# Performance work log

Hardware: AMD Instinct MI355X
Metric: run time of the kernel (lower is better)

## Reference

```python
import jax, jax.numpy as jnp
import numpy as np

B, L, DIM = 8, 512, 8          # batch, seq len, raw channels (value dim D = 2*DIM = 16)
ET, HID, H = 128, 128, 2       # embed_time, hidden_size, num_heads
MAXLEN = 512
NEG = -1e9


def setup_inputs() -> dict:
    key = jax.random.key(0)
    ks = jax.random.split(key, 40)
    def n(i, shape, s=0.05):
        return jax.random.normal(ks[i], shape, jnp.float32) * s
    vals = jax.random.normal(ks[0], (B, L, DIM), jnp.float32)
    msk = (jax.random.uniform(ks[1], (B, L, DIM)) > 0.2).astype(jnp.float32)
    x = jnp.concatenate([vals, msk], -1)                      # (B, L, 2*DIM)
    time_steps = jax.random.uniform(ks[2], (B, L), jnp.float32)
    return {
        'x': x, 'time_steps': time_steps,
        # learned time embedding: Linear(1, ET-1) periodic + Linear(1,1)
        'w_per': n(3, (1, ET - 1)), 'b_per': n(4, (ET - 1,)),
        'w_lin': n(5, (1, 1)), 'b_lin': n(6, (1,)),
        # MultiTimeAttention projections
        'Wq_t': n(7, (ET, ET)), 'bq_t': n(8, (ET,)),
        'Wk_t': n(9, (ET, ET)), 'bk_t': n(10, (ET,)),
        'Wo_t': n(11, (2 * DIM * H, HID)), 'bo_t': n(12, (HID,)),
        'pos_emb': n(13, (MAXLEN + 1, HID)), 'cls_emb': n(14, (1, HID)),
        # transformer block (BERT-style post-LN encoder layer, d_ff=HID)
        'tWq': n(15, (HID, HID)), 'tbq': n(16, (HID,)),
        'tWk': n(17, (HID, HID)), 'tbk': n(18, (HID,)),
        'tWv': n(19, (HID, HID)), 'tbv': n(20, (HID,)),
        'tWo': n(21, (HID, HID)), 'tbo': n(22, (HID,)),
        'ln1_g': jnp.ones((HID,), jnp.float32), 'ln1_b': jnp.zeros((HID,), jnp.float32),
        'fW1': n(23, (HID, HID)), 'fb1': n(24, (HID,)),
        'fW2': n(25, (HID, HID)), 'fb2': n(26, (HID,)),
        'ln2_g': jnp.ones((HID,), jnp.float32), 'ln2_b': jnp.zeros((HID,), jnp.float32),
        # BertPooler
        'pW': n(27, (HID, HID)), 'pb': n(28, (HID,)),
    }


def _time_emb(tt, w_per, b_per, w_lin, b_lin):
    tt = tt[..., None]                                        # (B, L, 1)
    return jnp.concatenate([tt @ w_lin + b_lin, jnp.sin(tt @ w_per + b_per)], -1)


def _ln(x, g, b, eps=1e-5):
    m = x.mean(-1, keepdims=True)
    v = ((x - m) ** 2).mean(-1, keepdims=True)
    return (x - m) / jnp.sqrt(v + eps) * g + b


def _mta(q_emb, k_emb, value, mask, Wq, bq, Wk, bk, Wo, bo):
    # MultiTimeAttention: scores broadcast to value-channel axis, softmax over keys
    D = value.shape[-1]
    dk = ET // H
    def split(e, W, b):
        p = e @ W + b
        return p.reshape(e.shape[0], -1, H, dk).transpose(0, 2, 1, 3)
    q = split(q_emb, Wq, bq)                                  # (Bq, H, Lq, dk)
    k = split(k_emb, Wk, bk)                                  # (B,  H, Lk, dk)
    scores = jnp.matmul(q, k.swapaxes(-1, -2)) / jnp.sqrt(jnp.float32(dk))  # (B,H,Lq,Lk)
    s5 = jnp.where(mask[:, None, None, :, :] == 0, NEG, scores[..., None])  # (B,H,Lq,Lk,D)
    p = jax.nn.softmax(s5, axis=-2)
    out = jnp.einsum('bhqkd,bkd->bhqd', p, value)             # (B, H, Lq, D)
    Bv = value.shape[0]
    out = out.transpose(0, 2, 1, 3).reshape(Bv, -1, H * D)
    return out @ Wo + bo


def _tblock(x, tWq, tbq, tWk, tbk, tWv, tbv, tWo, tbo, ln1_g, ln1_b,
            fW1, fb1, fW2, fb2, ln2_g, ln2_b):
    Bq, Lq, _ = x.shape
    dk = HID // H
    def heads(W, b):
        return (x @ W + b).reshape(Bq, Lq, H, dk).transpose(0, 2, 1, 3)
    q, k, v = heads(tWq, tbq), heads(tWk, tbk), heads(tWv, tbv)
    a = jax.nn.softmax(jnp.matmul(q, k.swapaxes(-1, -2)) / jnp.sqrt(jnp.float32(dk)), -1)
    o = jnp.matmul(a, v).transpose(0, 2, 1, 3).reshape(Bq, Lq, HID) @ tWo + tbo
    x = _ln(x + o, ln1_g, ln1_b)
    f = jax.nn.relu(x @ fW1 + fb1) @ fW2 + fb2
    return _ln(x + f, ln2_g, ln2_b)


def reference(x, time_steps, w_per, b_per, w_lin, b_lin,
              Wq_t, bq_t, Wk_t, bk_t, Wo_t, bo_t, pos_emb, cls_emb,
              tWq, tbq, tWk, tbk, tWv, tbv, tWo, tbo, ln1_g, ln1_b,
              fW1, fb1, fW2, fb2, ln2_g, ln2_b, pW, pb):
    Bx = x.shape[0]
    mask_half = x[:, :, DIM:]
    mask = jnp.concatenate([mask_half, mask_half], -1)        # (B, L, 2*DIM)
    key_e = _time_emb(time_steps, w_per, b_per, w_lin, b_lin)
    tq_e = _time_emb(time_steps, w_per, b_per, w_lin, b_lin)  # query_time_steps=None -> same
    cls_t = jnp.linspace(0.0, 1.0, 128, dtype=jnp.float32)[None]
    cls_q_e = _time_emb(cls_t, w_per, b_per, w_lin, b_lin)    # (1, 128, ET)
    cls_out = _mta(cls_q_e, key_e, x, mask, Wq_t, bq_t, Wk_t, bk_t, Wo_t, bo_t)
    out = _mta(tq_e, key_e, x, mask, Wq_t, bq_t, Wk_t, bk_t, Wo_t, bo_t)
    tb = (tWq, tbq, tWk, tbk, tWv, tbv, tWo, tbo, ln1_g, ln1_b,
          fW1, fb1, fW2, fb2, ln2_g, ln2_b)
    cls_repr = jnp.broadcast_to(cls_emb[None, :, :], (Bx, 1, HID))
    # encode(cls_out, is_pooling=True), pooling='bert': no pos emb, take token 0
    h = _tblock(jnp.concatenate([cls_repr, cls_out], 1), *tb)
    cls_pooling = jnp.tanh(h[:, 0] @ pW + pb)                 # (B, HID)
    # encode(out, is_pooling=False) [pretrain path]: pos emb + transformer, drop CLS
    h2 = jnp.concatenate([cls_repr, out], 1)                  # (B, L+1, HID)
    h2 = h2 + pos_emb[:h2.shape[1]][None]
    h2 = _tblock(h2, *tb)
    last_hidden_state = h2[:, 1:]                             # (B, L, HID)
    return cls_pooling, last_hidden_state
```

## Files before the change

kernel.cpp:

```cpp
#include <hip/hip_runtime.h>
#include <hip/hip_bf16.h>
#include <math.h>


static constexpr int NM_ = 8 * 513;
static constexpr int NC_ = 8 * 129;
static constexpr int NT_ = NM_ + NC_;
static constexpr int VTS_ = 5248;

using bf = __hip_bfloat16;
typedef __attribute__((ext_vector_type(8))) short bf16x8;
typedef __attribute__((ext_vector_type(4))) short bf16x4;
typedef __attribute__((ext_vector_type(4))) float floatx4;
typedef __attribute__((ext_vector_type(8))) unsigned short ushortx8;

__device__ __forceinline__ float wave_reduce_sum(float v) {
    #pragma unroll
    for (int off = 32; off >= 1; off >>= 1) v += __shfl_xor(v, off);
    return v;
}
__device__ __forceinline__ float wave_reduce_max(float v) {
    #pragma unroll
    for (int off = 32; off >= 1; off >>= 1) v = fmaxf(v, __shfl_xor(v, off));
    return v;
}
__device__ __forceinline__ float u2f(unsigned short u) {
    return __uint_as_float(((unsigned)u) << 16);
}
__device__ __forceinline__ unsigned short f2u(float f) {
    unsigned u = __float_as_uint(f);
    return (unsigned short)((u + 0x7FFF + ((u >> 16) & 1)) >> 16);
}
__device__ __forceinline__ bf16x8 join8(bf16x4 lo, bf16x4 hi) {
    return __builtin_shufflevector(lo, hi, 0, 1, 2, 3, 4, 5, 6, 7);
}
__device__ __forceinline__ float rdin(const void* p, int i, int flag) {
    return flag ? u2f(((const unsigned short*)p)[i]) : ((const float*)p)[i];
}

struct PrepAll {
    const void* src[32]; int n[32]; int dstoff[32];
    int cstart[32]; int cnum[32];
    int ncv;
    const void* wsrc[8]; unsigned short* wdst[8]; float wscale[8];
    const void* ts; const void* w_per; const void* b_per;
    const void* w_lin; const void* b_lin;
    unsigned short* key_e16;
    unsigned short* btg;
    const void* xsrc;
    unsigned short* vt;
    const unsigned short* det;
};
__global__ void prep_all_kernel(PrepAll a, float* dst) {
    int flag = (a.det[0] == 0x3F80u) ? 1 : 0;
    int blk = blockIdx.x, tid = threadIdx.x;
    if (blk < a.ncv) {
        int which = -1, bi = 0;
        #pragma unroll
        for (int i = 0; i < 32; ++i)
            if (blk >= a.cstart[i] && blk < a.cstart[i] + a.cnum[i]) { which = i; bi = blk - a.cstart[i]; }
        if (which < 0) return;
        int i = bi * 256 + tid;
        if (i < a.n[which]) dst[a.dstoff[which] + i] = rdin(a.src[which], i, flag);
    } else if (blk < a.ncv + 512) {
        int p = blk - a.ncv;
        int m = p >> 6;
        int idx = (p & 63) * 256 + tid;
        int c = idx >> 9;
        int l = (idx >> 3) & 63;
        int j = idx & 7;
        int k = (c >> 3) * 32 + (l >> 4) * 8 + j;
        int n = (c & 7) * 16 + (l & 15);
        a.wdst[m][idx] = f2u(rdin(a.wsrc[m], k * 128 + n, flag) * a.wscale[m]);
    } else if (blk < a.ncv + 512 + 2112) {
        int p = blk - a.ncv - 512;
        int row = p * 2 + (tid >> 7), j = tid & 127;
        float t = (row < 4096) ? rdin(a.ts, row, flag)
                               : (float)(row - 4096) * (1.0f / 127.0f);
        float v;
        if (j == 0) v = t * rdin(a.w_lin, 0, flag) + rdin(a.b_lin, 0, flag);
        else        v = sinf(t * rdin(a.w_per, j - 1, flag) + rdin(a.b_per, j - 1, flag));
        a.key_e16[row * 128 + j] = f2u(v);
    } else if (blk < a.ncv + 512 + 2112 + 32) {
        int p = blk - a.ncv - 512 - 2112;
        int e0 = (p * 256 + tid) * 8;
        int b = e0 >> 13;
        int c = (e0 >> 9) & 15;
        int k0 = e0 & 511;
        unsigned short out[8];
        #pragma unroll
        for (int j = 0; j < 8; ++j) {
            int k = k0 + j;
            float m = rdin(a.xsrc, (b * 512 + k) * 16 + 8 + (c & 7), flag);
            float val = (c < 8) ? rdin(a.xsrc, (b * 512 + k) * 16 + c, flag) * m : m;
            out[j] = f2u(val);
        }
        *(ushortx8*)(a.btg + e0) = *(ushortx8*)out;
    } else {
        int p = blk - a.ncv - 512 - 2112 - 32;
        int idx = p * 256 + tid;
        if (idx < 128 * 14) {
            int n = idx / 14, c8 = idx - n * 14;
            ushortx8 z = {0, 0, 0, 0, 0, 0, 0, 0};
            *(ushortx8*)(a.vt + (size_t)n * VTS_ + 5136 + c8 * 8) = z;
        }
    }
}

struct GemmM {
    const void* A[3]; const unsigned short* W[3]; const float* bias[3];
    unsigned short* C[3];
    int M[3]; float bscale[3];
};
__global__ void __launch_bounds__(256)
gemm_mfma_kernel(GemmM p) {
    int y = blockIdx.y;
    const unsigned short* Wsw = p.W[y];
    const float* bias = p.bias[y];
    unsigned short* C = p.C[y];
    int M = p.M[y];
    float bscale = p.bscale[y];
    int m0 = blockIdx.x * 16;
    if (m0 >= M) return;
    int tid = threadIdx.x;
    int wv = tid >> 6, lane = tid & 63;
    int am = lane & 15, aq = lane >> 4;
    const unsigned short* A = (const unsigned short*)p.A[y];
    const unsigned short* Arow = A + (size_t)(m0 + am) * 128;
    floatx4 acc0 = {0.f, 0.f, 0.f, 0.f}, acc1 = acc0;
    #pragma unroll
    for (int ks = 0; ks < 4; ++ks) {
        bf16x8 af = *(const bf16x8*)(Arow + ks * 32 + aq * 8);
        const unsigned short* base = Wsw + ((size_t)ks * 8 + 2 * wv) * 512 + lane * 8;
        bf16x8 b0 = *(const bf16x8*)(base);
        bf16x8 b1 = *(const bf16x8*)(base + 512);
        acc0 = __builtin_amdgcn_mfma_f32_16x16x32_bf16(af, b0, acc0, 0, 0, 0);
        acc1 = __builtin_amdgcn_mfma_f32_16x16x32_bf16(af, b1, acc1, 0, 0, 0);
    }
    int col = lane & 15, rowb = (lane >> 4) * 4;
    #pragma unroll
    for (int t = 0; t < 2; ++t) {
        floatx4 acc = t ? acc1 : acc0;
        int n = wv * 32 + t * 16 + col;
        float bv = bias[n] * bscale;
        #pragma unroll
        for (int rg = 0; rg < 4; ++rg)
            C[(size_t)(m0 + rowb + rg) * 128 + n] = f2u(acc[rg] + bv);
    }
}

struct MaU_att { unsigned short sp[16][520]; float red[1280]; };
struct MaU_qkv { unsigned short As[16][136]; };
union MaU { MaU_att att; MaU_qkv qkv; };

__global__ void __launch_bounds__(256)
mta_fused_kernel(const unsigned short* qp_cls, const unsigned short* qp_main,
                 const unsigned short* kp, const unsigned short* btg,
                 const float* Wo, const float* bo, const float* cls_emb, const float* pos,
                 float* xin,
                 const unsigned short* Wq, const unsigned short* Wk, const unsigned short* Wv,
                 const float* bq, const float* bk, const float* bv_,
                 unsigned short* outq, unsigned short* outk, unsigned short* vT) {
    __shared__ MaU U;
    __shared__ float As32[16][36];
    int vb = blockIdx.x, tid = threadIdx.x;
    int lane = tid & 63, wv = tid >> 6;
    int m = lane & 15, g = lane >> 4;
    bool special = (vb == 320);
    int is_cls = 0, qt = 0, b = 0;
    if (!special) {
        if (vb < 256) { b = vb >> 5; qt = vb & 31; }
        else { int t = vb - 256; b = t >> 3; qt = t & 7; is_cls = 1; }
    }
    int q0 = qt * 16;

    if (!special) {
        for (int h = 0; h < 2; ++h) {
            const unsigned short* qrow = is_cls
                ? (qp_cls + (size_t)(q0 + m) * 128 + h * 64)
                : (qp_main + (size_t)(b * 512 + q0 + m) * 128 + h * 64);
            bf16x8 qf0 = *(const bf16x8*)(qrow + g * 8);
            bf16x8 qf1 = *(const bf16x8*)(qrow + 32 + g * 8);

            const unsigned short* kbase = kp + ((size_t)b * 512) * 128 + h * 64;
            #pragma unroll
            for (int kt = 0; kt < 8; ++kt) {
                int colk = kt * 64 + wv * 16 + m;
                const unsigned short* kb = kbase + (size_t)colk * 128;
                bf16x8 b0 = *(const bf16x8*)(kb + g * 8);
                bf16x8 b1 = *(const bf16x8*)(kb + 32 + g * 8);
                floatx4 acc = {0.f, 0.f, 0.f, 0.f};
                acc = __builtin_amdgcn_mfma_f32_16x16x32_bf16(qf0, b0, acc, 0, 0, 0);
                acc = __builtin_amdgcn_mfma_f32_16x16x32_bf16(qf1, b1, acc, 0, 0, 0);
                #pragma unroll
                for (int rg = 0; rg < 4; ++rg) U.att.sp[g * 4 + rg][colk] = f2u(acc[rg]);
            }
            __syncthreads();

            for (int rr = wv; rr < 16; rr += 4) {
                float mx = -1e30f;
                for (int k = lane; k < 512; k += 64) mx = fmaxf(mx, u2f(U.att.sp[rr][k]));
                mx = wave_reduce_max(mx);
                for (int k = lane; k < 512; k += 64)
                    U.att.sp[rr][k] = f2u(expf(u2f(U.att.sp[rr][k]) - mx));
            }
            __syncthreads();

            floatx4 macc = {0.f, 0.f, 0.f, 0.f};
            {
                const unsigned short* bbase = btg + ((size_t)(b * 16 + m)) * 512 + g * 8;
                #pragma unroll
                for (int cc = 0; cc < 4; ++cc) {
                    int koff = (wv + cc * 4) * 32;
                    bf16x8 af = *(const bf16x8*)&U.att.sp[m][koff + g * 8];
                    bf16x8 bfv = *(const bf16x8*)(bbase + koff);
                    macc = __builtin_amdgcn_mfma_f32_16x16x32_bf16(af, bfv, macc, 0, 0, 0);
                }
            }
            float* redC = U.att.red;
            float* Cfull = U.att.red + 1024;
            #pragma unroll
            for (int rg = 0; rg < 4; ++rg) redC[tid * 4 + rg] = macc[rg];
            __syncthreads();
            {
                int l = tid >> 2, rg = tid & 3;
                float s = redC[l * 4 + rg] + redC[(64 + l) * 4 + rg]
                        + redC[(128 + l) * 4 + rg] + redC[(192 + l) * 4 + rg];
                int row = (l >> 4) * 4 + rg, c = l & 15;
                Cfull[row * 16 + c] = s;
            }
            __syncthreads();
            if (tid < 128) {
                int r = tid >> 3, c = tid & 7;
                float num = Cfull[r * 16 + c];
                float den = Cfull[r * 16 + 8 + c];
                As32[r][h * 16 + c] = num / den;
                As32[r][h * 16 + 8 + c] = 1.0f;
            }
            __syncthreads();
        }
    }

    int r = tid >> 4, gi = tid & 15, c0 = gi * 8;
    int segbase = is_cls ? (NM_ + b * 129) : (b * 513);
    auto Rof = [&](int rr) -> int {
        if (special) return (rr < 8) ? rr * 513 : NM_ + (rr - 8) * 129;
        return segbase + 1 + q0 + rr;
    };
    int R = Rof(r);
    int prow;
    if (special) prow = (r < 8) ? 0 : -1;
    else prow = is_cls ? -1 : (1 + q0 + r);

    float acc[8];
    if (special) {
        #pragma unroll
        for (int j = 0; j < 8; ++j) acc[j] = cls_emb[c0 + j];
    } else {
        #pragma unroll
        for (int j = 0; j < 8; ++j) acc[j] = bo[c0 + j];
        #pragma unroll 8
        for (int k = 0; k < 32; ++k) {
            float a = As32[r][k];
            const float4 w0 = *(const float4*)(Wo + (size_t)k * 128 + c0);
            const float4 w1 = *(const float4*)(Wo + (size_t)k * 128 + c0 + 4);
            acc[0] = fmaf(a, w0.x, acc[0]); acc[1] = fmaf(a, w0.y, acc[1]);
            acc[2] = fmaf(a, w0.z, acc[2]); acc[3] = fmaf(a, w0.w, acc[3]);
            acc[4] = fmaf(a, w1.x, acc[4]); acc[5] = fmaf(a, w1.y, acc[5]);
            acc[6] = fmaf(a, w1.z, acc[6]); acc[7] = fmaf(a, w1.w, acc[7]);
        }
    }
    if (prow >= 0) {
        const float* pr = pos + (size_t)prow * 128 + c0;
        float4 p0 = *(const float4*)(pr);
        float4 p1 = *(const float4*)(pr + 4);
        acc[0] += p0.x; acc[1] += p0.y; acc[2] += p0.z; acc[3] += p0.w;
        acc[4] += p1.x; acc[5] += p1.y; acc[6] += p1.z; acc[7] += p1.w;
    }
    *(float4*)(xin + (size_t)R * 128 + c0) = make_float4(acc[0], acc[1], acc[2], acc[3]);
    *(float4*)(xin + (size_t)R * 128 + c0 + 4) = make_float4(acc[4], acc[5], acc[6], acc[7]);
    *(ushort4*)&U.qkv.As[r][c0] = make_ushort4(f2u(acc[0]), f2u(acc[1]), f2u(acc[2]), f2u(acc[3]));
    *(ushort4*)&U.qkv.As[r][c0 + 4] = make_ushort4(f2u(acc[4]), f2u(acc[5]), f2u(acc[6]), f2u(acc[7]));
    __syncthreads();

    int am = lane & 15, aq = lane >> 4;
    int col = lane & 15, rowb = (lane >> 4) * 4;
    const unsigned short* Ws[3] = {Wq, Wk, Wv};
    const float* bs[3] = {bq, bk, bv_};
    float bsc[3] = {0.125f, 1.f, 1.f};
    unsigned short* Cs[2] = {outq, outk};
    #pragma unroll
    for (int y = 0; y < 3; ++y) {
        floatx4 acc0 = {0.f, 0.f, 0.f, 0.f}, acc1 = acc0;
        #pragma unroll
        for (int ks = 0; ks < 4; ++ks) {
            bf16x8 af = *(bf16x8*)&U.qkv.As[am][ks * 32 + aq * 8];
            const unsigned short* base = Ws[y] + ((size_t)ks * 8 + 2 * wv) * 512 + lane * 8;
            bf16x8 b0 = *(const bf16x8*)(base);
            bf16x8 b1 = *(const bf16x8*)(base + 512);
            acc0 = __builtin_amdgcn_mfma_f32_16x16x32_bf16(af, b0, acc0, 0, 0, 0);
            acc1 = __builtin_amdgcn_mfma_f32_16x16x32_bf16(af, b1, acc1, 0, 0, 0);
        }
        #pragma unroll
        for (int t = 0; t < 2; ++t) {
            floatx4 a2 = t ? acc1 : acc0;
            int n = wv * 32 + t * 16 + col;
            float bvv = bs[y][n] * bsc[y];
            #pragma unroll
            for (int rg = 0; rg < 4; ++rg) {
                unsigned short val = f2u(a2[rg] + bvv);
                int R2 = Rof(rowb + rg);
                if (y < 2) Cs[y][(size_t)R2 * 128 + n] = val;
                else       vT[(size_t)n * VTS_ + R2] = val;
            }
        }
    }
}

struct TbU_att { unsigned short sp[16][588]; };
struct TbU_ffn { float Xs[16][128]; unsigned short Hs[16][136]; };
union TbU { TbU_att att; TbU_ffn ffn; };

__global__ void __launch_bounds__(256)
tb_fused_kernel(const unsigned short* qp, const unsigned short* kp,
                const unsigned short* vT, const float* resid,
                const unsigned short* Wao, const float* bao,
                const float* g1, const float* b1ln,
                const unsigned short* W1, const float* fb1,
                const unsigned short* W2, const float* fb2,
                const float* g2, const float* b2ln,
                const float* pW, const float* pb, float* dout) {
    __shared__ TbU U;
    __shared__ unsigned short As[16][136];
    __shared__ float rinv[16];
    __shared__ float redS[4][4][4], redQ[4][4][4], smean[16], sinv[16], x2row[128];
    __shared__ int poolb;

    int xx = blockIdx.x, b = blockIdx.y, tid = threadIdx.x;
    int is_cls = (xx >= 33);
    int qt = is_cls ? xx - 33 : xx;
    int Lq = is_cls ? 129 : 513;
    int base = is_cls ? (NM_ + b * 129) : (b * 513);
    int nkt = is_cls ? 3 : 9;
    int lane = tid & 63, wv = tid >> 6;
    int q0 = qt * 16, m = lane & 15, g = lane >> 4;
    if (tid == 0) poolb = -1;

    for (int h = 0; h < 2; ++h) {
        int qr = q0 + m; if (qr >= Lq) qr = Lq - 1;
        const unsigned short* qrow = qp + (size_t)(base + qr) * 128 + h * 64;
        bf16x8 qf0 = *(const bf16x8*)(qrow + g * 8);
        bf16x8 qf1 = *(const bf16x8*)(qrow + 32 + g * 8);

        for (int kt = 0; kt < nkt; ++kt) {
            int colk = kt * 64 + wv * 16 + m;
            int krow = (colk < Lq) ? colk : (Lq - 1);
            const unsigned short* kb = kp + (size_t)(base + krow) * 128 + h * 64;
            bf16x8 b0 = *(const bf16x8*)(kb + g * 8);
            bf16x8 b1 = *(const bf16x8*)(kb + 32 + g * 8);
            floatx4 acc = {0.f, 0.f, 0.f, 0.f};
            acc = __builtin_amdgcn_mfma_f32_16x16x32_bf16(qf0, b0, acc, 0, 0, 0);
            acc = __builtin_amdgcn_mfma_f32_16x16x32_bf16(qf1, b1, acc, 0, 0, 0);
            #pragma unroll
            for (int rg = 0; rg < 4; ++rg)
                U.att.sp[g * 4 + rg][colk] = f2u((colk < Lq) ? acc[rg] : -1e30f);
        }
        __syncthreads();

        int kend = nkt * 64;
        for (int rr = wv; rr < 16; rr += 4) {
            float mx = -1e30f;
            for (int k = lane; k < kend; k += 64) mx = fmaxf(mx, u2f(U.att.sp[rr][k]));
            mx = wave_reduce_max(mx);
            float sum = 0.f;
            for (int k = lane; k < kend; k += 64) {
                float e = expf(u2f(U.att.sp[rr][k]) - mx);
                U.att.sp[rr][k] = f2u(e);
                sum += e;
            }
            sum = wave_reduce_sum(sum);
            if (lane == 0) rinv[rr] = 1.f / sum;
        }
        __syncthreads();

        floatx4 oacc = {0.f, 0.f, 0.f, 0.f};
        const unsigned short* vbase = vT + (size_t)(h * 64 + wv * 16 + m) * VTS_ + base;
        for (int kt = 0; kt < nkt; ++kt) {
            int k0 = kt * 64;
            #pragma unroll
            for (int c = 0; c < 2; ++c) {
                bf16x4 plo = *(const bf16x4*)&U.att.sp[m][k0 + c * 32 + g * 8];
                bf16x4 phi = *(const bf16x4*)&U.att.sp[m][k0 + c * 32 + g * 8 + 4];
                bf16x8 vf = *(const bf16x8*)(vbase + k0 + c * 32 + g * 8);
                oacc = __builtin_amdgcn_mfma_f32_16x16x32_bf16(join8(plo, phi), vf, oacc, 0, 0, 0);
            }
        }
        int dcol = wv * 16 + m;
        #pragma unroll
        for (int rg = 0; rg < 4; ++rg) {
            int q = g * 4 + rg;
            As[q][h * 64 + dcol] = f2u(oacc[rg] * rinv[q]);
        }
        __syncthreads();
    }

    int am = lane & 15, aq = lane >> 4;
    int col = lane & 15, rowb = g * 4;

    float ov[2][4];
    {
        floatx4 acc0 = {0.f, 0.f, 0.f, 0.f}, acc1 = acc0;
        #pragma unroll
        for (int ks = 0; ks < 4; ++ks) {
            bf16x8 af = *(bf16x8*)&As[am][ks * 32 + aq * 8];
            const unsigned short* wb = Wao + ((size_t)ks * 8 + 2 * wv) * 512 + lane * 8;
            bf16x8 bb0 = *(const bf16x8*)(wb);
            bf16x8 bb1 = *(const bf16x8*)(wb + 512);
            acc0 = __builtin_amdgcn_mfma_f32_16x16x32_bf16(af, bb0, acc0, 0, 0, 0);
            acc1 = __builtin_amdgcn_mfma_f32_16x16x32_bf16(af, bb1, acc1, 0, 0, 0);
        }
        #pragma unroll
        for (int t = 0; t < 2; ++t) {
            int n = wv * 32 + t * 16 + col;
            float bv = bao[n];
            floatx4 acc = t ? acc1 : acc0;
            #pragma unroll
            for (int rg = 0; rg < 4; ++rg) {
                int qo = q0 + rowb + rg;
                int rc = (qo < Lq) ? qo : (Lq - 1);
                ov[t][rg] = acc[rg] + bv + resid[(size_t)(base + rc) * 128 + n];
            }
        }
    }
    #pragma unroll
    for (int rg = 0; rg < 4; ++rg) {
        float s = ov[0][rg] + ov[1][rg];
        float q = ov[0][rg] * ov[0][rg] + ov[1][rg] * ov[1][rg];
        #pragma unroll
        for (int off = 8; off >= 1; off >>= 1) {
            s += __shfl_xor(s, off);
            q += __shfl_xor(q, off);
        }
        if ((lane & 15) == 0) { redS[wv][g][rg] = s; redQ[wv][g][rg] = q; }
    }
    __syncthreads();
    if (tid < 16) {
        int gg = tid >> 2, rg = tid & 3;
        float s = redS[0][gg][rg] + redS[1][gg][rg] + redS[2][gg][rg] + redS[3][gg][rg];
        float q = redQ[0][gg][rg] + redQ[1][gg][rg] + redQ[2][gg][rg] + redQ[3][gg][rg];
        float mean = s * 0.0078125f;
        float var = q * 0.0078125f - mean * mean;
        smean[tid] = mean;
        sinv[tid] = rsqrtf(var + 1e-5f);
    }
    __syncthreads();
    #pragma unroll
    for (int t = 0; t < 2; ++t) {
        int n = wv * 32 + t * 16 + col;
        float gm = g1[n], bb = b1ln[n];
        #pragma unroll
        for (int rg = 0; rg < 4; ++rg) {
            int row = rowb + rg;
            float val = (ov[t][rg] - smean[row]) * sinv[row] * gm + bb;
            U.ffn.Xs[row][n] = val;
            As[row][n] = f2u(val);
        }
    }
    __syncthreads();

    {
        floatx4 acc0 = {0.f, 0.f, 0.f, 0.f}, acc1 = acc0;
        #pragma unroll
        for (int ks = 0; ks < 4; ++ks) {
            bf16x8 af = *(bf16x8*)&As[am][ks * 32 + aq * 8];
            const unsigned short* wb = W1 + ((size_t)ks * 8 + 2 * wv) * 512 + lane * 8;
            bf16x8 bb0 = *(const bf16x8*)(wb);
            bf16x8 bb1 = *(const bf16x8*)(wb + 512);
            acc0 = __builtin_amdgcn_mfma_f32_16x16x32_bf16(af, bb0, acc0, 0, 0, 0);
            acc1 = __builtin_amdgcn_mfma_f32_16x16x32_bf16(af, bb1, acc1, 0, 0, 0);
        }
        #pragma unroll
        for (int t = 0; t < 2; ++t) {
            int n = wv * 32 + t * 16 + col;
            float bv = fb1[n];
            floatx4 acc = t ? acc1 : acc0;
            #pragma unroll
            for (int rg = 0; rg < 4; ++rg)
                U.ffn.Hs[rowb + rg][n] = f2u(fmaxf(acc[rg] + bv, 0.f));
        }
    }
    __syncthreads();

    floatx4 acc0 = {0.f, 0.f, 0.f, 0.f}, acc1 = acc0;
    #pragma unroll
    for (int ks = 0; ks < 4; ++ks) {
        bf16x8 af = *(bf16x8*)&U.ffn.Hs[am][ks * 32 + aq * 8];
        const unsigned short* wb = W2 + ((size_t)ks * 8 + 2 * wv) * 512 + lane * 8;
        bf16x8 bb0 = *(const bf16x8*)(wb);
        bf16x8 bb1 = *(const bf16x8*)(wb + 512);
        acc0 = __builtin_amdgcn_mfma_f32_16x16x32_bf16(af, bb0, acc0, 0, 0, 0);
        acc1 = __builtin_amdgcn_mfma_f32_16x16x32_bf16(af, bb1, acc1, 0, 0, 0);
    }
    #pragma unroll
    for (int t = 0; t < 2; ++t) {
        int n = wv * 32 + t * 16 + col;
        float bv = fb2[n];
        floatx4 acc = t ? acc1 : acc0;
        #pragma unroll
        for (int rg = 0; rg < 4; ++rg)
            ov[t][rg] = acc[rg] + bv + U.ffn.Xs[rowb + rg][n];
    }
    #pragma unroll
    for (int rg = 0; rg < 4; ++rg) {
        float s = ov[0][rg] + ov[1][rg];
        float q = ov[0][rg] * ov[0][rg] + ov[1][rg] * ov[1][rg];
        #pragma unroll
        for (int off = 8; off >= 1; off >>= 1) {
            s += __shfl_xor(s, off);
            q += __shfl_xor(q, off);
        }
        if ((lane & 15) == 0) { redS[wv][g][rg] = s; redQ[wv][g][rg] = q; }
    }
    __syncthreads();
    if (tid < 16) {
        int gg = tid >> 2, rg = tid & 3;
        float s = redS[0][gg][rg] + redS[1][gg][rg] + redS[2][gg][rg] + redS[3][gg][rg];
        float q = redQ[0][gg][rg] + redQ[1][gg][rg] + redQ[2][gg][rg] + redQ[3][gg][rg];
        float mean = s * 0.0078125f;
        float var = q * 0.0078125f - mean * mean;
        smean[tid] = mean;
        sinv[tid] = rsqrtf(var + 1e-5f);
    }
    __syncthreads();
    #pragma unroll
    for (int t = 0; t < 2; ++t) {
        int n = wv * 32 + t * 16 + col;
        float gm = g2[n], bb = b2ln[n];
        #pragma unroll
        for (int rg = 0; rg < 4; ++rg) {
            int row = rowb + rg;
            int qout = q0 + row;
            float val = (ov[t][rg] - smean[row]) * sinv[row] * gm + bb;
            if (!is_cls) {
                if (qout >= 1 && qout < Lq)
                    dout[1024 + (size_t)b * 65536 + (size_t)(qout - 1) * 128 + n] = val;
            } else {
                if (qout == 0) {
                    x2row[n] = val;
                    if (n == 0) poolb = b;
                }
            }
        }
    }
    __syncthreads();
    if (poolb >= 0 && tid < 128) {
        float acc = pb[tid];
        for (int k = 0; k < 128; ++k) acc = fmaf(x2row[k], pW[(size_t)k * 128 + tid], acc);
        dout[(size_t)poolb * 128 + tid] = tanhf(acc);
    }
}

extern "C" void kernel_launch(void* const* d_in, const int* in_sizes, int n_in,
                              void* d_out, int out_size, void* d_ws, size_t ws_size,
                              hipStream_t stream) {
    float* w = (float*)d_ws;
    size_t off = 0;
    auto alloc = [&](size_t n) {
        float* p = w + off;
        off += (n + 3) & ~(size_t)3;
        return p;
    };
    auto allocU = [&](size_t n) { return (unsigned short*)alloc((n + 1) / 2); };

    PrepAll pa{};
    int nn = n_in < 32 ? n_in : 32;
    float* fin[32];
    const int needconv[32] = {0,0,0,0,0,0, 0,1, 0,1, 1,1, 1,1, 0,1, 0,1, 0,1,
                              0,1, 1,1, 0,1, 0,1, 1,1, 1,1};
    int ncv = 0;
    for (int i = 0; i < nn; ++i) {
        pa.src[i] = d_in[i];
        pa.n[i] = in_sizes[i];
        fin[i] = alloc(in_sizes[i]);
        pa.dstoff[i] = (int)(fin[i] - w);
        if (needconv[i]) {
            int nb = (in_sizes[i] + 255) / 256;
            pa.cstart[i] = ncv;
            pa.cnum[i] = nb;
            ncv += nb;
        } else { pa.cstart[i] = -1; pa.cnum[i] = 0; }
    }
    for (int i = nn; i < 32; ++i) {
        pa.src[i] = nullptr; pa.n[i] = 0; pa.dstoff[i] = 0;
        pa.cstart[i] = -1; pa.cnum[i] = 0;
    }
    pa.ncv = ncv;

    const float* bq_t    = fin[7];
    const float* bk_t    = fin[9];
    const float* Wo_t    = fin[10]; const float* bo_t = fin[11];
    const float* pos_emb = fin[12]; const float* cls_emb = fin[13];
    const float* tbq = fin[15]; const float* tbk = fin[17]; const float* tbv = fin[19];
    const float* tbo = fin[21];
    const float* ln1_g = fin[22]; const float* ln1_b = fin[23];
    const float* fb1 = fin[25]; const float* fb2 = fin[27];
    const float* ln2_g = fin[28]; const float* ln2_b = fin[29];
    const float* pW = fin[30]; const float* pb = fin[31];

    const int widx[8] = {8, 6, 14, 16, 18, 20, 24, 26};
    unsigned short* wsw[8];
    for (int i = 0; i < 8; ++i) {
        wsw[i] = allocU(16384);
        pa.wsrc[i] = d_in[widx[i]];
        pa.wdst[i] = wsw[i];
        pa.wscale[i] = (i == 1 || i == 2) ? 0.125f : 1.0f;
    }
    pa.ts = d_in[1]; pa.w_per = d_in[2]; pa.b_per = d_in[3];
    pa.w_lin = d_in[4]; pa.b_lin = d_in[5];
    pa.xsrc = d_in[0];
    pa.det = (const unsigned short*)d_in[22];

    unsigned short* key_e16 = allocU(4224 * 128);
    unsigned short* cls_e16 = key_e16 + 4096 * 128;
    pa.key_e16 = key_e16;
    unsigned short* btg = allocU(8 * 16 * 512);
    pa.btg = btg;

    unsigned short* qp_main16 = allocU(4096 * 128);
    unsigned short* kp_main16 = allocU(4096 * 128);
    unsigned short* qp_cls16  = allocU(128 * 128);
    float* xin     = alloc((size_t)NT_ * 128);
    unsigned short* tbq16 = allocU((size_t)NT_ * 128);
    unsigned short* tbk16 = allocU((size_t)NT_ * 128);
    unsigned short* vT    = allocU((size_t)128 * VTS_);
    pa.vt = vT;
    (void)ws_size;

    float* outf = (float*)d_out;
    int prep_nblk = ncv + 512 + 2112 + 32 + 7;

    prep_all_kernel<<<prep_nblk, 256, 0, stream>>>(pa, w);

    {
        GemmM p{};
        p.A[0] = key_e16; p.W[0] = wsw[0]; p.bias[0] = bk_t; p.C[0] = kp_main16;
        p.M[0] = 4096; p.bscale[0] = 1.f;
        p.A[1] = key_e16; p.W[1] = wsw[1]; p.bias[1] = bq_t; p.C[1] = qp_main16;
        p.M[1] = 4096; p.bscale[1] = 0.125f;
        p.A[2] = cls_e16; p.W[2] = wsw[1]; p.bias[2] = bq_t; p.C[2] = qp_cls16;
        p.M[2] = 128; p.bscale[2] = 0.125f;
        gemm_mfma_kernel<<<dim3(256, 3), 256, 0, stream>>>(p);
    }

    mta_fused_kernel<<<321, 256, 0, stream>>>(qp_cls16, qp_main16, kp_main16, btg,
                                              Wo_t, bo_t, cls_emb, pos_emb, xin,
                                              wsw[2], wsw[3], wsw[4], tbq, tbk, tbv,
                                              tbq16, tbk16, vT);

    tb_fused_kernel<<<dim3(42, 8), 256, 0, stream>>>(tbq16, tbk16, vT, xin,
                                                     wsw[5], tbo, ln1_g, ln1_b,
                                                     wsw[6], fb1, wsw[7], fb2,
                                                     ln2_g, ln2_b, pW, pb, outf);
}
```

Measured before the change: 207.3 us.

## Process both attention heads together to halve barriers in fused attention kernels

Both the MTA and transformer-block attention phases now compute scores, softmax and PV products for the two heads at once, using doubled shared-memory score buffers instead of a sequential per-head loop. This cuts the number of __syncthreads per block roughly in half and exposes more independent MFMA/load work for latency hiding. The transformer path becomes templated on key-tile count, so its loops fully unroll, and both kernels add a min-blocks-per-CU launch bound of 2. The cost is larger shared memory and register use per block, which could reduce occupancy despite the launch-bound hint.

```diff
diff --git a/kernel.cpp b/kernel.cpp
--- a/kernel.cpp
+++ b/kernel.cpp
@@ -149,11 +149,10 @@
     }
 }
 
-struct MaU_att { unsigned short sp[16][520]; float red[1280]; };
-struct MaU_qkv { unsigned short As[16][136]; };
-union MaU { MaU_att att; MaU_qkv qkv; };
-
-__global__ void __launch_bounds__(256)
+struct MaAtt { unsigned short sp[2][16][520]; float red[2][1280]; };
+union MaU { MaAtt att; unsigned short qAs[16][136]; };
+
+__global__ void __launch_bounds__(256, 2)
 mta_fused_kernel(const unsigned short* qp_cls, const unsigned short* qp_main,
                  const unsigned short* kp, const unsigned short* btg,
                  const float* Wo, const float* bo, const float* cls_emb, const float* pos,
@@ -175,70 +174,89 @@
     int q0 = qt * 16;
 
     if (!special) {
+        const unsigned short* qrow = is_cls
+            ? (qp_cls + (size_t)(q0 + m) * 128)
+            : (qp_main + (size_t)(b * 512 + q0 + m) * 128);
+        bf16x8 qf[2][2];
+        #pragma unroll
         for (int h = 0; h < 2; ++h) {
-            const unsigned short* qrow = is_cls
-                ? (qp_cls + (size_t)(q0 + m) * 128 + h * 64)
-                : (qp_main + (size_t)(b * 512 + q0 + m) * 128 + h * 64);
-            bf16x8 qf0 = *(const bf16x8*)(qrow + g * 8);
-            bf16x8 qf1 = *(const bf16x8*)(qrow + 32 + g * 8);
-
-            const unsigned short* kbase = kp + ((size_t)b * 512) * 128 + h * 64;
-            #pragma unroll
-            for (int kt = 0; kt < 8; ++kt) {
-                int colk = kt * 64 + wv * 16 + m;
-                const unsigned short* kb = kbase + (size_t)colk * 128;
-                bf16x8 b0 = *(const bf16x8*)(kb + g * 8);
-                bf16x8 b1 = *(const bf16x8*)(kb + 32 + g * 8);
+            qf[h][0] = *(const bf16x8*)(qrow + h * 64 + g * 8);
+            qf[h][1] = *(const bf16x8*)(qrow + h * 64 + 32 + g * 8);
+        }
+        const unsigned short* kbase = kp + ((size_t)b * 512) * 128;
+        #pragma unroll
+        for (int kt = 0; kt < 8; ++kt) {
+            int colk = kt * 64 + wv * 16 + m;
+            const unsigned short* kb = kbase + (size_t)colk * 128;
+            #pragma unroll
+            for (int h = 0; h < 2; ++h) {
+                bf16x8 b0 = *(const bf16x8*)(kb + h * 64 + g * 8);
+                bf16x8 b1 = *(const bf16x8*)(kb + h * 64 + 32 + g * 8);
                 floatx4 acc = {0.f, 0.f, 0.f, 0.f};
-                acc = __builtin_amdgcn_mfma_f32_16x16x32_bf16(qf0, b0, acc, 0, 0, 0);
-                acc = __builtin_amdgcn_mfma_f32_16x16x32_bf16(qf1, b1, acc, 0, 0, 0);
+                acc = __builtin_amdgcn_mfma_f32_16x16x32_bf16(qf[h][0], b0, acc, 0, 0, 0);
+                acc = __builtin_amdgcn_mfma_f32_16x16x32_bf16(qf[h][1], b1, acc, 0, 0, 0);
                 #pragma unroll
-                for (int rg = 0; rg < 4; ++rg) U.att.sp[g * 4 + rg][colk] = f2u(acc[rg]);
+                for (int rg = 0; rg < 4; ++rg)
+                    U.att.sp[h][g * 4 + rg][colk] = f2u(acc[rg]);
             }
-            __syncthreads();
-
-            for (int rr = wv; rr < 16; rr += 4) {
-                float mx = -1e30f;
-                for (int k = lane; k < 512; k += 64) mx = fmaxf(mx, u2f(U.att.sp[rr][k]));
-                mx = wave_reduce_max(mx);
-                for (int k = lane; k < 512; k += 64)
-                    U.att.sp[rr][k] = f2u(expf(u2f(U.att.sp[rr][k]) - mx));
-            }
-            __syncthreads();
-
-            floatx4 macc = {0.f, 0.f, 0.f, 0.f};
-            {
-                const unsigned short* bbase = btg + ((size_t)(b * 16 + m)) * 512 + g * 8;
+        }
+        __syncthreads();
+
+        for (int rr2 = wv; rr2 < 32; rr2 += 4) {
+            int h = rr2 >> 4, rr = rr2 & 15;
+            float mx = -1e30f;
+            #pragma unroll
+            for (int k = 0; k < 8; ++k) mx = fmaxf(mx, u2f(U.att.sp[h][rr][k * 64 + lane]));
+            mx = wave_reduce_max(mx);
+            #pragma unroll
+            for (int k = 0; k < 8; ++k)
+                U.att.sp[h][rr][k * 64 + lane] = f2u(expf(u2f(U.att.sp[h][rr][k * 64 + lane]) - mx));
+        }
+        __syncthreads();
+
+        floatx4 macc[2] = {{0.f,0.f,0.f,0.f},{0.f,0.f,0.f,0.f}};
+        {
+            const unsigned short* bbase = btg + ((size_t)(b * 16 + m)) * 512 + g * 8;
+            #pragma unroll
+            for (int cc = 0; cc < 4; ++cc) {
+                int koff = (wv + cc * 4) * 32;
+                bf16x8 bfv = *(const bf16x8*)(bbase + koff);
                 #pragma unroll
-                for (int cc = 0; cc < 4; ++cc) {
-                    int koff = (wv + cc * 4) * 32;
-                    bf16x8 af = *(const bf16x8*)&U.att.sp[m][koff + g * 8];
-                    bf16x8 bfv = *(const bf16x8*)(bbase + koff);
-                    macc = __builtin_amdgcn_mfma_f32_16x16x32_bf16(af, bfv, macc, 0, 0, 0);
+                for (int h = 0; h < 2; ++h) {
+                    bf16x8 af = *(const bf16x8*)&U.att.sp[h][m][koff + g * 8];
+                    macc[h] = __builtin_amdgcn_mfma_f32_16x16x32_bf16(af, bfv, macc[h], 0, 0, 0);
                 }
             }
-            float* redC = U.att.red;
-            float* Cfull = U.att.red + 1024;
-            #pragma unroll
-            for (int rg = 0; rg < 4; ++rg) redC[tid * 4 + rg] = macc[rg];
-            __syncthreads();
-            {
-                int l = tid >> 2, rg = tid & 3;
-                float s = redC[l * 4 + rg] + redC[(64 + l) * 4 + rg]
-                        + redC[(128 + l) * 4 + rg] + redC[(192 + l) * 4 + rg];
-                int row = (l >> 4) * 4 + rg, c = l & 15;
-                Cfull[row * 16 + c] = s;
+        }
+        #pragma unroll
+        for (int h = 0; h < 2; ++h)
+            #pragma unroll
+            for (int rg = 0; rg < 4; ++rg)
+                U.att.red[h][tid * 4 + rg] = macc[h][rg];
+        __syncthreads();
+        {
+            int l = tid >> 2, rg = tid & 3;
+            int row = (l >> 4) * 4 + rg, c = l & 15;
+            #pragma unroll
+            for (int h = 0; h < 2; ++h) {
+                const float* rc = U.att.red[h];
+                float s = rc[l * 4 + rg] + rc[(64 + l) * 4 + rg]
+                        + rc[(128 + l) * 4 + rg] + rc[(192 + l) * 4 + rg];
+                U.att.red[h][1024 + row * 16 + c] = s;
             }
-            __syncthreads();
-            if (tid < 128) {
-                int r = tid >> 3, c = tid & 7;
-                float num = Cfull[r * 16 + c];
-                float den = Cfull[r * 16 + 8 + c];
+        }
+        __syncthreads();
+        if (tid < 128) {
+            int r = tid >> 3, c = tid & 7;
+            #pragma unroll
+            for (int h = 0; h < 2; ++h) {
+                float num = U.att.red[h][1024 + r * 16 + c];
+                float den = U.att.red[h][1024 + r * 16 + 8 + c];
                 As32[r][h * 16 + c] = num / den;
                 As32[r][h * 16 + 8 + c] = 1.0f;
             }
-            __syncthreads();
-        }
+        }
+        __syncthreads();
     }
 
     int r = tid >> 4, gi = tid & 15, c0 = gi * 8;
@@ -277,10 +295,11 @@
         acc[0] += p0.x; acc[1] += p0.y; acc[2] += p0.z; acc[3] += p0.w;
         acc[4] += p1.x; acc[5] += p1.y; acc[6] += p1.z; acc[7] += p1.w;
     }
+    __syncthreads();
     *(float4*)(xin + (size_t)R * 128 + c0) = make_float4(acc[0], acc[1], acc[2], acc[3]);
     *(float4*)(xin + (size_t)R * 128 + c0 + 4) = make_float4(acc[4], acc[5], acc[6], acc[7]);
-    *(ushort4*)&U.qkv.As[r][c0] = make_ushort4(f2u(acc[0]), f2u(acc[1]), f2u(acc[2]), f2u(acc[3]));
-    *(ushort4*)&U.qkv.As[r][c0 + 4] = make_ushort4(f2u(acc[4]), f2u(acc[5]), f2u(acc[6]), f2u(acc[7]));
+    *(ushort4*)&U.qAs[r][c0] = make_ushort4(f2u(acc[0]), f2u(acc[1]), f2u(acc[2]), f2u(acc[3]));
+    *(ushort4*)&U.qAs[r][c0 + 4] = make_ushort4(f2u(acc[4]), f2u(acc[5]), f2u(acc[6]), f2u(acc[7]));
     __syncthreads();
 
     int am = lane & 15, aq = lane >> 4;
@@ -294,7 +313,7 @@
         floatx4 acc0 = {0.f, 0.f, 0.f, 0.f}, acc1 = acc0;
         #pragma unroll
         for (int ks = 0; ks < 4; ++ks) {
-            bf16x8 af = *(bf16x8*)&U.qkv.As[am][ks * 32 + aq * 8];
+            bf16x8 af = *(bf16x8*)&U.qAs[am][ks * 32 + aq * 8];
             const unsigned short* base = Ws[y] + ((size_t)ks * 8 + 2 * wv) * 512 + lane * 8;
             bf16x8 b0 = *(const bf16x8*)(base);
             bf16x8 b1 = *(const bf16x8*)(base + 512);
@@ -317,11 +336,95 @@
     }
 }
 
-struct TbU_att { unsigned short sp[16][588]; };
-struct TbU_ffn { float Xs[16][128]; unsigned short Hs[16][136]; };
-union TbU { TbU_att att; TbU_ffn ffn; };
-
-__global__ void __launch_bounds__(256)
+union TbU {
+    unsigned short sp[2][16][588];
+    struct { float Xs[16][128]; unsigned short Hs[16][136]; } ffn;
+};
+
+template<int NKT>
+__device__ __forceinline__ void tb_attn_phase(
+    const unsigned short* qp, const unsigned short* kp, const unsigned short* vT,
+    int Lq, int base, int q0, int tid,
+    unsigned short (&sp)[2][16][588], float (&rinv)[2][16],
+    unsigned short (&As)[16][136])
+{
+    int lane = tid & 63, wv = tid >> 6;
+    int m = lane & 15, g = lane >> 4;
+
+    int qr = q0 + m; if (qr >= Lq) qr = Lq - 1;
+    const unsigned short* qrow = qp + (size_t)(base + qr) * 128;
+    bf16x8 qf[2][2];
+    #pragma unroll
+    for (int h = 0; h < 2; ++h) {
+        qf[h][0] = *(const bf16x8*)(qrow + h * 64 + g * 8);
+        qf[h][1] = *(const bf16x8*)(qrow + h * 64 + 32 + g * 8);
+    }
+
+    #pragma unroll
+    for (int kt = 0; kt < NKT; ++kt) {
+        int colk = kt * 64 + wv * 16 + m;
+        int krow = (colk < Lq) ? colk : (Lq - 1);
+        const unsigned short* kb = kp + (size_t)(base + krow) * 128;
+        #pragma unroll
+        for (int h = 0; h < 2; ++h) {
+            bf16x8 b0 = *(const bf16x8*)(kb + h * 64 + g * 8);
+            bf16x8 b1 = *(const bf16x8*)(kb + h * 64 + 32 + g * 8);
+            floatx4 acc = {0.f, 0.f, 0.f, 0.f};
+            acc = __builtin_amdgcn_mfma_f32_16x16x32_bf16(qf[h][0], b0, acc, 0, 0, 0);
+            acc = __builtin_amdgcn_mfma_f32_16x16x32_bf16(qf[h][1], b1, acc, 0, 0, 0);
+            #pragma unroll
+            for (int rg = 0; rg < 4; ++rg)
+                sp[h][g * 4 + rg][colk] = f2u((colk < Lq) ? acc[rg] : -1e30f);
+        }
+    }
+    __syncthreads();
+
+    for (int rr2 = wv; rr2 < 32; rr2 += 4) {
+        int h = rr2 >> 4, rr = rr2 & 15;
+        float mx = -1e30f;
+        #pragma unroll
+        for (int k = 0; k < NKT; ++k) mx = fmaxf(mx, u2f(sp[h][rr][k * 64 + lane]));
+        mx = wave_reduce_max(mx);
+        float sum = 0.f;
+        #pragma unroll
+        for (int k = 0; k < NKT; ++k) {
+            float e = expf(u2f(sp[h][rr][k * 64 + lane]) - mx);
+            sp[h][rr][k * 64 + lane] = f2u(e);
+            sum += e;
+        }
+        sum = wave_reduce_sum(sum);
+        if (lane == 0) rinv[h][rr] = 1.f / sum;
+    }
+    __syncthreads();
+
+    floatx4 oacc[2] = {{0.f,0.f,0.f,0.f},{0.f,0.f,0.f,0.f}};
+    #pragma unroll
+    for (int kt = 0; kt < NKT; ++kt) {
+        int k0 = kt * 64;
+        #pragma unroll
+        for (int h = 0; h < 2; ++h) {
+            const unsigned short* vbase = vT + (size_t)(h * 64 + wv * 16 + m) * VTS_ + base;
+            #pragma unroll
+            for (int c = 0; c < 2; ++c) {
+                bf16x4 plo = *(const bf16x4*)&sp[h][m][k0 + c * 32 + g * 8];
+                bf16x4 phi = *(const bf16x4*)&sp[h][m][k0 + c * 32 + g * 8 + 4];
+                bf16x8 vf = *(const bf16x8*)(vbase + k0 + c * 32 + g * 8);
+                oacc[h] = __builtin_amdgcn_mfma_f32_16x16x32_bf16(join8(plo, phi), vf, oacc[h], 0, 0, 0);
+            }
+        }
+    }
+    int dcol = wv * 16 + m;
+    #pragma unroll
+    for (int h = 0; h < 2; ++h)
+        #pragma unroll
+        for (int rg = 0; rg < 4; ++rg) {
+            int q = g * 4 + rg;
+            As[q][h * 64 + dcol] = f2u(oacc[h][rg] * rinv[h][q]);
+        }
+    __syncthreads();
+}
+
+__global__ void __launch_bounds__(256, 2)
 tb_fused_kernel(const unsigned short* qp, const unsigned short* kp,
                 const unsigned short* vT, const float* resid,
                 const unsigned short* Wao, const float* bao,
@@ -332,7 +435,7 @@
                 const float* pW, const float* pb, float* dout) {
     __shared__ TbU U;
     __shared__ unsigned short As[16][136];
-    __shared__ float rinv[16];
+    __shared__ float rinv[2][16];
     __shared__ float redS[4][4][4], redQ[4][4][4], smean[16], sinv[16], x2row[128];
     __shared__ int poolb;
 
@@ -341,68 +444,12 @@
     int qt = is_cls ? xx - 33 : xx;
     int Lq = is_cls ? 129 : 513;
     int base = is_cls ? (NM_ + b * 129) : (b * 513);
-    int nkt = is_cls ? 3 : 9;
     int lane = tid & 63, wv = tid >> 6;
-    int q0 = qt * 16, m = lane & 15, g = lane >> 4;
+    int q0 = qt * 16, g = lane >> 4;
     if (tid == 0) poolb = -1;
 
-    for (int h = 0; h < 2; ++h) {
-        int qr = q0 + m; if (qr >= Lq) qr = Lq - 1;
-        const unsigned short* qrow = qp + (size_t)(base + qr) * 128 + h * 64;
-        bf16x8 qf0 = *(const bf16x8*)(qrow + g * 8);
-        bf16x8 qf1 = *(const bf16x8*)(qrow + 32 + g * 8);
-
-        for (int kt = 0; kt < nkt; ++kt) {
-            int colk = kt * 64 + wv * 16 + m;
-            int krow = (colk < Lq) ? colk : (Lq - 1);
-            const unsigned short* kb = kp + (size_t)(base + krow) * 128 + h * 64;
-            bf16x8 b0 = *(const bf16x8*)(kb + g * 8);
-            bf16x8 b1 = *(const bf16x8*)(kb + 32 + g * 8);
-            floatx4 acc = {0.f, 0.f, 0.f, 0.f};
-            acc = __builtin_amdgcn_mfma_f32_16x16x32_bf16(qf0, b0, acc, 0, 0, 0);
-            acc = __builtin_amdgcn_mfma_f32_16x16x32_bf16(qf1, b1, acc, 0, 0, 0);
-            #pragma unroll
-            for (int rg = 0; rg < 4; ++rg)
-                U.att.sp[g * 4 + rg][colk] = f2u((colk < Lq) ? acc[rg] : -1e30f);
-        }
-        __syncthreads();
-
-        int kend = nkt * 64;
-        for (int rr = wv; rr < 16; rr += 4) {
-            float mx = -1e30f;
-            for (int k = lane; k < kend; k += 64) mx = fmaxf(mx, u2f(U.att.sp[rr][k]));
-            mx = wave_reduce_max(mx);
-            float sum = 0.f;
-            for (int k = lane; k < kend; k += 64) {
-                float e = expf(u2f(U.att.sp[rr][k]) - mx);
-                U.att.sp[rr][k] = f2u(e);
-                sum += e;
-            }
-            sum = wave_reduce_sum(sum);
-            if (lane == 0) rinv[rr] = 1.f / sum;
-        }
-        __syncthreads();
-
-        floatx4 oacc = {0.f, 0.f, 0.f, 0.f};
-        const unsigned short* vbase = vT + (size_t)(h * 64 + wv * 16 + m) * VTS_ + base;
-        for (int kt = 0; kt < nkt; ++kt) {
-            int k0 = kt * 64;
-            #pragma unroll
-            for (int c = 0; c < 2; ++c) {
-                bf16x4 plo = *(const bf16x4*)&U.att.sp[m][k0 + c * 32 + g * 8];
-                bf16x4 phi = *(const bf16x4*)&U.att.sp[m][k0 + c * 32 + g * 8 + 4];
-                bf16x8 vf = *(const bf16x8*)(vbase + k0 + c * 32 + g * 8);
-                oacc = __builtin_amdgcn_mfma_f32_16x16x32_bf16(join8(plo, phi), vf, oacc, 0, 0, 0);
-            }
-        }
-        int dcol = wv * 16 + m;
-        #pragma unroll
-        for (int rg = 0; rg < 4; ++rg) {
-            int q = g * 4 + rg;
-            As[q][h * 64 + dcol] = f2u(oacc[rg] * rinv[q]);
-        }
-        __syncthreads();
-    }
+    if (is_cls) tb_attn_phase<3>(qp, kp, vT, Lq, base, q0, tid, U.sp, rinv, As);
+    else        tb_attn_phase<9>(qp, kp, vT, Lq, base, q0, tid, U.sp, rinv, As);
 
     int am = lane & 15, aq = lane >> 4;
     int col = lane & 15, rowb = g * 4;
```

Measured after the change: 203.9 us. No clear change (-1.6%).
